# Kernel optimization log

Hardware: AMD Instinct MI355X
Metric: run time of the kernel (lower is better)

## Reference

```python
import jax, jax.numpy as jnp
import numpy as np

N, E, F_IN, F_OUT = 8192, 1024, 256, 256


def setup_inputs() -> dict:
    key = jax.random.key(0)
    k1, k2, k3, k4 = jax.random.split(key, 4)
    X = jax.random.normal(k1, (N, F_IN), dtype=jnp.float32)
    # binary incidence matrix: node i belongs to hyperedge j with p=0.05
    H = (jax.random.uniform(k2, (N, E)) < 0.05).astype(jnp.float32)
    W = jax.random.normal(k3, (F_OUT, F_IN), dtype=jnp.float32) * (1.0 / np.sqrt(F_IN))
    b = jax.random.normal(k4, (F_OUT,), dtype=jnp.float32) * 0.01
    return {"X": X, "H": H, "W": W, "b": b}


def reference(X, H, W, b):
    # Dv = diag(row sums of H), De = diag(col sums of H)
    dv = jnp.sum(H, axis=1)                      # [N] node degrees
    de = jnp.sum(H, axis=0)                      # [E] edge degrees
    dv_inv_sqrt = 1.0 / jnp.sqrt(dv)             # inv of sqrt(Dv) (diagonal)
    de_inv = 1.0 / de                            # inv of De (diagonal)
    # diagonal matrices realized as broadcast scalings (same math, no N x N).
    Xs = X * dv_inv_sqrt[:, None]
    M = H.T @ Xs                                 # H^T (...)          [E, F]
    M = M * de_inv[:, None]                      # De^-1 (...)        [E, F]
    X_new = (H @ M) * dv_inv_sqrt[:, None]       # Dv^-1/2 H (...)    [N, F]
    return X_new @ W.T + b                       # nn.Linear
```

## Files before the change

### kernel.cpp

```cpp
#include <hip/hip_runtime.h>
#include <hip/hip_bf16.h>
#include <stdint.h>

typedef __attribute__((ext_vector_type(8))) short bf16x8;
typedef __attribute__((ext_vector_type(4))) float f32x4;
typedef __attribute__((ext_vector_type(4))) unsigned int u32x4;
typedef __attribute__((ext_vector_type(2))) unsigned int u32x2;
typedef unsigned short u16;
typedef unsigned int u32;
typedef unsigned char u8;
typedef unsigned long long u64;

#define N_NODES 8192
#define N_EDGES 1024
#define F_DIM   256
#define NMAX 128

__device__ __forceinline__ u16 f2bf(float f) {
    union { float f; u32 u; } v; v.f = f;
    u32 u = v.u;
    u = (u + 0x7FFFu + ((u >> 16) & 1u)) >> 16;
    return (u16)u;
}
__device__ __forceinline__ float bflo(u32 p) {
    union { u32 u; float f; } v; v.u = p << 16; return v.f;
}
__device__ __forceinline__ float bfhi(u32 p) {
    union { u32 u; float f; } v; v.u = p & 0xffff0000u; return v.f;
}

__device__ __forceinline__ void async16(const u16* g, u16* l) {
    __builtin_amdgcn_global_load_lds(
        (const __attribute__((address_space(1))) u32*)(const void*)g,
        (__attribute__((address_space(3))) u32*)(void*)l, 16, 0, 0);
}

__device__ __forceinline__ bf16x8 expand8(u32 byte) {
    union { u32 u[4]; bf16x8 v; } r;
#pragma unroll
    for (int i = 0; i < 4; ++i)
        r.u[i] = (((byte >> (2 * i)) & 1u) ? 0x3F80u : 0u)
               | (((byte >> (2 * i + 1)) & 1u) ? 0x3F800000u : 0u);
    return r.v;
}

__global__ __launch_bounds__(512) void prep(
    const float* __restrict__ H, const float* __restrict__ X,
    const float* __restrict__ W,
    float* __restrict__ dv, u16* __restrict__ nlist,
    u16* __restrict__ Xst, u32* __restrict__ HbTs, u16* __restrict__ Wb) {
    __shared__ u16 hmask[32][64];
    __shared__ u16 tT[256][34];
    const int tid = threadIdx.x;
    const int wv = tid >> 6;
    const int lane = tid & 63;
    const int blk = blockIdx.x;
    const int n0 = blk * 32 + wv * 4;

    f32x4 hv[4][4], xv[4];
#pragma unroll
    for (int r = 0; r < 4; ++r) {
        const int n = n0 + r;
#pragma unroll
        for (int q = 0; q < 4; ++q)
            hv[r][q] = *(const f32x4*)(&H[(size_t)n * N_EDGES + q * 256 + lane * 4]);
        xv[r] = *(const f32x4*)(&X[(size_t)n * F_DIM + lane * 4]);
    }

    if (wv == 7) {
        const f32x4 w = *(const f32x4*)(&W[(size_t)blk * F_DIM + lane * 4]);
        u32x2 pk;
        pk[0] = (u32)f2bf(w[0]) | ((u32)f2bf(w[1]) << 16);
        pk[1] = (u32)f2bf(w[2]) | ((u32)f2bf(w[3]) << 16);
        *(u32x2*)(&Wb[(size_t)blk * F_DIM + lane * 4]) = pk;
    }

#pragma unroll
    for (int r = 0; r < 4; ++r) {
        const int n = n0 + r;
        u32 m16 = 0u;
#pragma unroll
        for (int q = 0; q < 4; ++q)
#pragma unroll
            for (int j = 0; j < 4; ++j)
                m16 |= ((hv[r][q][j] != 0.f) ? 1u : 0u) << (q * 4 + j);
        hmask[wv * 4 + r][lane] = (u16)m16;
        const u32 cl = (u32)__popc(m16);
        u32 x = cl;
#pragma unroll
        for (int d = 1; d < 64; d <<= 1) {
            const u32 t = __shfl_up(x, d, 64);
            if (lane >= d) x += t;
        }
        const u32 total = __shfl(x, 63, 64);
        u32 pos = x - cl;
        u16* nrow = &nlist[(size_t)n * NMAX];
        u32 m = m16;
        while (m) {
            const int bidx = __builtin_ctz(m);
            m &= m - 1;
            const int col = ((bidx >> 2) << 8) + lane * 4 + (bidx & 3);
            if (pos < NMAX) nrow[pos] = (u16)col;
            ++pos;
        }
        if (lane == 0) dv[n] = (float)total;
        const float s = rsqrtf((float)total);
#pragma unroll
        for (int j = 0; j < 4; ++j)
            tT[lane * 4 + j][wv * 4 + r] = f2bf(xv[r][j] * s);
    }
    __syncthreads();
    {
        u32x2 st;
#pragma unroll
        for (int eo = 0; eo < 2; ++eo) {
            const int e = tid * 2 + eo;
            const int widx = (e & 255) >> 2;
            const int bit = ((e >> 8) << 2) + (e & 3);
            u32 w = 0u;
#pragma unroll
            for (int r = 0; r < 32; ++r)
                w |= (u32)((hmask[r][widx] >> bit) & 1u) << r;
            st[eo] = w;
        }
        *(u32x2*)(&HbTs[(size_t)blk * N_EDGES + tid * 2]) = st;
    }
    {
        const int f = tid & 255, half = tid >> 8;
        const u32* src = (const u32*)(&tT[f][half * 16]);
        u32x4 a, b2;
#pragma unroll
        for (int i = 0; i < 4; ++i) { a[i] = src[i]; b2[i] = src[i + 4]; }
        u16* dst = &Xst[(size_t)f * N_NODES + blk * 32 + half * 16];
        *(u32x4*)dst = a;
        *(u32x4*)(dst + 8) = b2;
    }
}

__global__ __launch_bounds__(512) void gemm1(
    const u16* __restrict__ Xst, const u32* __restrict__ HbTs,
    u16* __restrict__ Mb) {
    __shared__ __align__(16) u8 smem[65536];
    __shared__ float cnts[8][2][16];
    const int tid = threadIdx.x;
    const int wv = tid >> 6, lane = tid & 63;
    const int f0 = ((int)blockIdx.x & 7) * 32;
    const int e0 = ((int)blockIdx.x >> 3) * 32;
    const int row16 = lane & 15, quad = lane >> 4;
    const int srow = lane & 15, schunk = lane >> 4;
    u16* myBs = (u16*)(smem + wv * 8192);
    const int kbase = wv * 1024;

    f32x4 acc[2][2] = {};
    u32 cnt0 = 0, cnt1 = 0;
    u32 wA[2][2], wB[2][2];

    auto STAGE = [&](int it, int buf) {
        __builtin_amdgcn_sched_barrier(0);
        const int k0 = kbase + it * 64;
#pragma unroll
        for (int tn = 0; tn < 2; ++tn)
#pragma unroll
            for (int ks = 0; ks < 2; ++ks)
                async16(Xst + (size_t)(f0 + tn * 16 + srow) * N_NODES + k0 + ks * 32 + schunk * 8,
                        myBs + buf * 2048 + (tn * 2 + ks) * 512);
    };
    auto LOADW = [&](int it, u32 (&w)[2][2]) {
        const int k0 = kbase + it * 64;
#pragma unroll
        for (int tm = 0; tm < 2; ++tm)
#pragma unroll
            for (int ks = 0; ks < 2; ++ks)
                w[tm][ks] = HbTs[(size_t)((k0 >> 5) + ks) * N_EDGES + e0 + tm * 16 + row16];
    };
    auto COMPUTE = [&](int buf, u32 (&w)[2][2]) {
        asm volatile("s_waitcnt vmcnt(4)" ::: "memory");
        __builtin_amdgcn_sched_barrier(0);
#pragma unroll
        for (int ks = 0; ks < 2; ++ks) {
            bf16x8 bfr[2];
#pragma unroll
            for (int tn = 0; tn < 2; ++tn)
                bfr[tn] = *(const bf16x8*)(myBs + buf * 2048 + (tn * 2 + ks) * 512 + lane * 8);
#pragma unroll
            for (int tm = 0; tm < 2; ++tm) {
                const u32 byte = (w[tm][ks] >> (quad * 8)) & 0xFFu;
                if (tm == 0) cnt0 += (u32)__popc(byte); else cnt1 += (u32)__popc(byte);
                const bf16x8 af = expand8(byte);
#pragma unroll
                for (int tn = 0; tn < 2; ++tn)
                    acc[tm][tn] = __builtin_amdgcn_mfma_f32_16x16x32_bf16(
                        af, bfr[tn], acc[tm][tn], 0, 0, 0);
            }
        }
    };

    STAGE(0, 0);
    LOADW(0, wA);
    for (int i = 0; i < 8; ++i) {
        STAGE(2 * i + 1, 1);
        LOADW(2 * i + 1, wB);
        COMPUTE(0, wA);
        const int nxt = (2 * i + 2 < 16) ? (2 * i + 2) : 15;
        STAGE(nxt, 0);
        LOADW(nxt, wA);
        COMPUTE(1, wB);
    }

    cnt0 += __shfl_down(cnt0, 32, 64); cnt0 += __shfl_down(cnt0, 16, 64);
    cnt1 += __shfl_down(cnt1, 32, 64); cnt1 += __shfl_down(cnt1, 16, 64);
    if (lane < 16) {
        cnts[wv][0][lane] = (float)cnt0;
        cnts[wv][1][lane] = (float)cnt1;
    }
    __syncthreads();
    {
        float* redf = (float*)smem;
        float* my = &redf[(size_t)(wv * 64 + lane) * 17];
#pragma unroll
        for (int tm = 0; tm < 2; ++tm)
#pragma unroll
            for (int tn = 0; tn < 2; ++tn)
#pragma unroll
                for (int r = 0; r < 4; ++r)
                    my[tm * 8 + tn * 4 + r] = acc[tm][tn][r];
    }
    __syncthreads();
    {
        const float* redf = (const float*)smem;
#pragma unroll
        for (int h = 0; h < 2; ++h) {
            const int idx = tid + h * 512;
            const int el = idx >> 5, fl = idx & 31;
            const int tm = el >> 4, q = (el >> 2) & 3, r = el & 3;
            const int tn = fl >> 4, r16 = fl & 15;
            const int srcl = q * 16 + r16;
            const int j = tm * 8 + tn * 4 + r;
            float s = 0.f, de = 0.f;
#pragma unroll
            for (int w = 0; w < 8; ++w) {
                s += redf[(size_t)(w * 64 + srcl) * 17 + j];
                de += cnts[w][tm][el & 15];
            }
            Mb[(size_t)(e0 + el) * F_DIM + f0 + fl] = f2bf(s / de);
        }
    }
}

__global__ __launch_bounds__(512) void spmm2w(
    const u16* __restrict__ Mb, const float* __restrict__ dv,
    const u16* __restrict__ nlist, const u16* __restrict__ Wb,
    const float* __restrict__ bias, float* __restrict__ out) {
    __shared__ u16 nl[8 * NMAX];
    __shared__ u16 Yb[8][264];
    const int tid = threadIdx.x;
    const int wv = tid >> 6;
    const int lane = tid & 63;
    const int n0 = blockIdx.x * 8;
    ((u32*)nl)[tid] = ((const u32*)&nlist[(size_t)n0 * NMAX])[tid];
    __syncthreads();
    const int half = lane >> 5, l32 = lane & 31;
    const int n = n0 + wv;
    const float dvn = dv[n];
    const int cnt = min((int)dvn, NMAX);
    const u16* lt = &nl[wv * NMAX];
    float a[8] = {};
    const int npairs = (cnt + 1) >> 1;
#pragma unroll 8
    for (int p = 0; p < npairs; ++p) {
        const int idx0 = 2 * p + half;
        const int idx = min(idx0, cnt - 1);
        const float msk = (idx0 < cnt) ? 1.f : 0.f;
        const int e = lt[idx];
        const u32x4 pk = *(const u32x4*)(&Mb[(size_t)e * F_DIM + l32 * 8]);
        a[0] = fmaf(bflo(pk[0]), msk, a[0]); a[1] = fmaf(bfhi(pk[0]), msk, a[1]);
        a[2] = fmaf(bflo(pk[1]), msk, a[2]); a[3] = fmaf(bfhi(pk[1]), msk, a[3]);
        a[4] = fmaf(bflo(pk[2]), msk, a[4]); a[5] = fmaf(bfhi(pk[2]), msk, a[5]);
        a[6] = fmaf(bflo(pk[3]), msk, a[6]); a[7] = fmaf(bfhi(pk[3]), msk, a[7]);
    }
#pragma unroll
    for (int k = 0; k < 8; ++k) a[k] += __shfl_xor(a[k], 32, 64);
    const float s = rsqrtf(dvn);
    if (half == 0) {
        u32x4 pk;
        pk[0] = (u32)f2bf(a[0] * s) | ((u32)f2bf(a[1] * s) << 16);
        pk[1] = (u32)f2bf(a[2] * s) | ((u32)f2bf(a[3] * s) << 16);
        pk[2] = (u32)f2bf(a[4] * s) | ((u32)f2bf(a[5] * s) << 16);
        pk[3] = (u32)f2bf(a[6] * s) | ((u32)f2bf(a[7] * s) << 16);
        *(u32x4*)(&Yb[wv][l32 * 8]) = pk;
    }
    __syncthreads();
    const int row16 = lane & 15, quad = lane >> 4;
    f32x4 acc[2] = {};
    for (int ko = 0; ko < 256; ko += 32) {
        bf16x8 af = {};
        if (row16 < 8)
            af = *(const bf16x8*)(&Yb[row16][ko + quad * 8]);
#pragma unroll
        for (int tn = 0; tn < 2; ++tn) {
            const int j = wv * 32 + tn * 16 + row16;
            const bf16x8 bf = *(const bf16x8*)(&Wb[(size_t)j * F_DIM + ko + quad * 8]);
            acc[tn] = __builtin_amdgcn_mfma_f32_16x16x32_bf16(af, bf, acc[tn], 0, 0, 0);
        }
    }
#pragma unroll
    for (int tn = 0; tn < 2; ++tn) {
        const int col = wv * 32 + tn * 16 + row16;
        const float bc = bias[col];
#pragma unroll
        for (int r2 = 0; r2 < 4; ++r2) {
            const int row = quad * 4 + r2;
            if (row < 8)
                out[(size_t)(n0 + row) * F_DIM + col] = acc[tn][r2] + bc;
        }
    }
}

extern "C" void kernel_launch(void* const* d_in, const int* in_sizes, int n_in,
                              void* d_out, int out_size, void* d_ws, size_t ws_size,
                              hipStream_t stream) {
    (void)in_sizes; (void)n_in; (void)out_size; (void)ws_size;
    const float* X = (const float*)d_in[0];
    const float* H = (const float*)d_in[1];
    const float* W = (const float*)d_in[2];
    const float* b = (const float*)d_in[3];
    float* out = (float*)d_out;

    char* ws = (char*)d_ws;
    float* dv    = (float*)(ws);
    u32*   HbTs  = (u32*)(ws + 0x10000);
    u16*   nlist = (u16*)(ws + 0x110000);
    u16*   Xst   = (u16*)(ws + 0x310000);
    u16*   Mb    = (u16*)(ws + 0x710000);
    u16*   Wb    = (u16*)(ws + 0x790000);

    prep<<<256, 512, 0, stream>>>(H, X, W, dv, nlist, Xst, HbTs, Wb);
    gemm1<<<256, 512, 0, stream>>>(Xst, HbTs, Mb);
    spmm2w<<<N_NODES / 8, 512, 0, stream>>>(Mb, dv, nlist, Wb, b, out);
}
```

Measured before the change: 138.4 us.

## Reassociate linear layer before hypergraph propagation and replace gather SpMM with bitmask MFMA GEMM

The Linear weight is applied first (Z = W·Xs), so the two incidence products run on already-projected features. The final propagation becomes a dense MFMA GEMM over a node-major bit-packed incidence matrix instead of a per-node neighbor-list gather, and the neighbor-list construction in prep is removed. This adds a fourth kernel and an extra 8192x256 bf16 intermediate in exchange for regular, coalesced MFMA work and no degree cap in the second product.

```diff
diff --git a/kernel.cpp b/kernel.cpp
--- a/kernel.cpp
+++ b/kernel.cpp
@@ -14,7 +14,6 @@
 #define N_NODES 8192
 #define N_EDGES 1024
 #define F_DIM   256
-#define NMAX 128
 
 __device__ __forceinline__ u16 f2bf(float f) {
     union { float f; u32 u; } v; v.f = f;
@@ -22,12 +21,6 @@
     u = (u + 0x7FFFu + ((u >> 16) & 1u)) >> 16;
     return (u16)u;
 }
-__device__ __forceinline__ float bflo(u32 p) {
-    union { u32 u; float f; } v; v.u = p << 16; return v.f;
-}
-__device__ __forceinline__ float bfhi(u32 p) {
-    union { u32 u; float f; } v; v.u = p & 0xffff0000u; return v.f;
-}
 
 __device__ __forceinline__ void async16(const u16* g, u16* l) {
     __builtin_amdgcn_global_load_lds(
@@ -47,10 +40,9 @@
 __global__ __launch_bounds__(512) void prep(
     const float* __restrict__ H, const float* __restrict__ X,
     const float* __restrict__ W,
-    float* __restrict__ dv, u16* __restrict__ nlist,
-    u16* __restrict__ Xst, u32* __restrict__ HbTs, u16* __restrict__ Wb) {
-    __shared__ u16 hmask[32][64];
-    __shared__ u16 tT[256][34];
+    float* __restrict__ dv, u16* __restrict__ Xsb,
+    u32* __restrict__ HbTs, u32* __restrict__ HbN, u16* __restrict__ Wb) {
+    __shared__ u16 hmask[32][68];
     const int tid = threadIdx.x;
     const int wv = tid >> 6;
     const int lane = tid & 63;
@@ -85,29 +77,15 @@
             for (int j = 0; j < 4; ++j)
                 m16 |= ((hv[r][q][j] != 0.f) ? 1u : 0u) << (q * 4 + j);
         hmask[wv * 4 + r][lane] = (u16)m16;
-        const u32 cl = (u32)__popc(m16);
-        u32 x = cl;
-#pragma unroll
-        for (int d = 1; d < 64; d <<= 1) {
-            const u32 t = __shfl_up(x, d, 64);
-            if (lane >= d) x += t;
-        }
-        const u32 total = __shfl(x, 63, 64);
-        u32 pos = x - cl;
-        u16* nrow = &nlist[(size_t)n * NMAX];
-        u32 m = m16;
-        while (m) {
-            const int bidx = __builtin_ctz(m);
-            m &= m - 1;
-            const int col = ((bidx >> 2) << 8) + lane * 4 + (bidx & 3);
-            if (pos < NMAX) nrow[pos] = (u16)col;
-            ++pos;
-        }
-        if (lane == 0) dv[n] = (float)total;
-        const float s = rsqrtf((float)total);
-#pragma unroll
-        for (int j = 0; j < 4; ++j)
-            tT[lane * 4 + j][wv * 4 + r] = f2bf(xv[r][j] * s);
+        u32 s = (u32)__popc(m16);
+#pragma unroll
+        for (int d = 1; d < 64; d <<= 1) s += __shfl_xor(s, d, 64);
+        if (lane == 0) dv[n] = (float)s;
+        const float sc = rsqrtf((float)s);
+        u32x2 pk;
+        pk[0] = (u32)f2bf(xv[r][0] * sc) | ((u32)f2bf(xv[r][1] * sc) << 16);
+        pk[1] = (u32)f2bf(xv[r][2] * sc) | ((u32)f2bf(xv[r][3] * sc) << 16);
+        *(u32x2*)(&Xsb[(size_t)n * F_DIM + lane * 4]) = pk;
     }
     __syncthreads();
     {
@@ -126,20 +104,89 @@
         *(u32x2*)(&HbTs[(size_t)blk * N_EDGES + tid * 2]) = st;
     }
     {
-        const int f = tid & 255, half = tid >> 8;
-        const u32* src = (const u32*)(&tT[f][half * 16]);
-        u32x4 a, b2;
-#pragma unroll
-        for (int i = 0; i < 4; ++i) { a[i] = src[i]; b2[i] = src[i + 4]; }
-        u16* dst = &Xst[(size_t)f * N_NODES + blk * 32 + half * 16];
-        *(u32x4*)dst = a;
-        *(u32x4*)(dst + 8) = b2;
-    }
-}
-
-__global__ __launch_bounds__(512) void gemm1(
-    const u16* __restrict__ Xst, const u32* __restrict__ HbTs,
-    u16* __restrict__ Mb) {
+        const int r = tid & 31;
+        const int wec = tid >> 5;
+#pragma unroll
+        for (int wo = 0; wo < 2; ++wo) {
+            const int we = wec + wo * 16;
+            const int q = we >> 3, l0 = (we & 7) * 8;
+            const u32x2 a = *(const u32x2*)(&hmask[r][l0]);
+            const u32x2 b2 = *(const u32x2*)(&hmask[r][l0 + 4]);
+            const u32 sh = q * 4;
+            u32 w = ((a[0] >> sh) & 0xFu)
+                  | (((a[0] >> (16 + sh)) & 0xFu) << 4)
+                  | (((a[1] >> sh) & 0xFu) << 8)
+                  | (((a[1] >> (16 + sh)) & 0xFu) << 12)
+                  | (((b2[0] >> sh) & 0xFu) << 16)
+                  | (((b2[0] >> (16 + sh)) & 0xFu) << 20)
+                  | (((b2[1] >> sh) & 0xFu) << 24)
+                  | (((b2[1] >> (16 + sh)) & 0xFu) << 28);
+            HbN[(size_t)we * N_NODES + blk * 32 + r] = w;
+        }
+    }
+}
+
+__global__ __launch_bounds__(256) void gemmZ(
+    const u16* __restrict__ Wb, const u16* __restrict__ Xsb,
+    u16* __restrict__ Zt) {
+    __shared__ __align__(16) u16 As[64 * 64];
+    __shared__ __align__(16) u16 Bs[64 * 64];
+    const int tid = threadIdx.x;
+    const int lane = tid & 63;
+    const int wave = tid >> 6;
+    const int wm = wave >> 1, wn = wave & 1;
+    const int row16 = lane & 15;
+    const int quad = lane >> 4;
+    const int row0 = blockIdx.y * 64;
+    const int col0 = blockIdx.x * 64;
+    const int srow = lane >> 3;
+    const int scol = (lane & 7) * 8;
+    const u16* gA0 = Wb + (size_t)(row0 + wave * 16 + srow) * F_DIM + scol;
+    const u16* gB0 = Xsb + (size_t)(col0 + wave * 16 + srow) * F_DIM + scol;
+    const size_t rstep8 = (size_t)8 * F_DIM;
+    u16* lA0 = &As[(wave * 16) * 64];
+    u16* lB0 = &Bs[(wave * 16) * 64];
+
+    f32x4 acc[2][2] = {};
+    for (int k = 0; k < 256; k += 64) {
+        async16(gA0 + k, lA0);
+        async16(gA0 + k + rstep8, lA0 + 8 * 64);
+        async16(gB0 + k, lB0);
+        async16(gB0 + k + rstep8, lB0 + 8 * 64);
+        __syncthreads();
+#pragma unroll
+        for (int ks = 0; ks < 2; ++ks) {
+            bf16x8 af[2], bfr[2];
+#pragma unroll
+            for (int t = 0; t < 2; ++t) {
+                af[t]  = *(const bf16x8*)(&As[(wm * 32 + t * 16 + row16) * 64 + ks * 32 + quad * 8]);
+                bfr[t] = *(const bf16x8*)(&Bs[(wn * 32 + t * 16 + row16) * 64 + ks * 32 + quad * 8]);
+            }
+#pragma unroll
+            for (int tm = 0; tm < 2; tm++)
+#pragma unroll
+                for (int tn = 0; tn < 2; tn++)
+                    acc[tm][tn] = __builtin_amdgcn_mfma_f32_16x16x32_bf16(
+                        af[tm], bfr[tn], acc[tm][tn], 0, 0, 0);
+        }
+        __syncthreads();
+    }
+#pragma unroll
+    for (int tm = 0; tm < 2; tm++)
+#pragma unroll
+        for (int tn = 0; tn < 2; tn++) {
+            const int col = col0 + wn * 32 + tn * 16 + row16;
+#pragma unroll
+            for (int r = 0; r < 4; r++) {
+                const int row = row0 + wm * 32 + tm * 16 + quad * 4 + r;
+                Zt[(size_t)row * N_NODES + col] = f2bf(acc[tm][tn][r]);
+            }
+        }
+}
+
+__global__ __launch_bounds__(512) void gemmM2(
+    const u16* __restrict__ Zt, const u32* __restrict__ HbTs,
+    u16* __restrict__ M2t) {
     __shared__ __align__(16) u8 smem[65536];
     __shared__ float cnts[8][2][16];
     const int tid = threadIdx.x;
@@ -162,7 +209,7 @@
         for (int tn = 0; tn < 2; ++tn)
 #pragma unroll
             for (int ks = 0; ks < 2; ++ks)
-                async16(Xst + (size_t)(f0 + tn * 16 + srow) * N_NODES + k0 + ks * 32 + schunk * 8,
+                async16(Zt + (size_t)(f0 + tn * 16 + srow) * N_NODES + k0 + ks * 32 + schunk * 8,
                         myBs + buf * 2048 + (tn * 2 + ks) * 512);
     };
     auto LOADW = [&](int it, u32 (&w)[2][2]) {
@@ -231,7 +278,7 @@
 #pragma unroll
         for (int h = 0; h < 2; ++h) {
             const int idx = tid + h * 512;
-            const int el = idx >> 5, fl = idx & 31;
+            const int fl = idx >> 5, el = idx & 31;
             const int tm = el >> 4, q = (el >> 2) & 3, r = el & 3;
             const int tn = fl >> 4, r16 = fl & 15;
             const int srcl = q * 16 + r16;
@@ -242,78 +289,86 @@
                 s += redf[(size_t)(w * 64 + srcl) * 17 + j];
                 de += cnts[w][tm][el & 15];
             }
-            Mb[(size_t)(e0 + el) * F_DIM + f0 + fl] = f2bf(s / de);
-        }
-    }
-}
-
-__global__ __launch_bounds__(512) void spmm2w(
-    const u16* __restrict__ Mb, const float* __restrict__ dv,
-    const u16* __restrict__ nlist, const u16* __restrict__ Wb,
-    const float* __restrict__ bias, float* __restrict__ out) {
-    __shared__ u16 nl[8 * NMAX];
-    __shared__ u16 Yb[8][264];
+            M2t[(size_t)(f0 + fl) * N_EDGES + e0 + el] = f2bf(s / de);
+        }
+    }
+}
+
+__global__ __launch_bounds__(512) void gemmOUT(
+    const u16* __restrict__ M2t, const u32* __restrict__ HbN,
+    const float* __restrict__ dv, const float* __restrict__ bias,
+    float* __restrict__ out) {
+    __shared__ __align__(16) u16 Bs[32 * 1028];
     const int tid = threadIdx.x;
-    const int wv = tid >> 6;
-    const int lane = tid & 63;
-    const int n0 = blockIdx.x * 8;
-    ((u32*)nl)[tid] = ((const u32*)&nlist[(size_t)n0 * NMAX])[tid];
+    const int wv = tid >> 6, lane = tid & 63;
+    const int row16 = lane & 15, quad = lane >> 4;
+    const int j0 = ((int)blockIdx.x & 7) * 32;
+    const int ng = ((int)blockIdx.x >> 3) * 256 + wv * 32;
+
+#pragma unroll
+    for (int rr = 0; rr < 4; ++rr) {
+        const int jr = wv * 4 + rr;
+#pragma unroll
+        for (int c = 0; c < 2; ++c)
+            async16(M2t + (size_t)(j0 + jr) * N_EDGES + c * 512 + lane * 8,
+                    &Bs[jr * 1028 + c * 512]);
+    }
     __syncthreads();
-    const int half = lane >> 5, l32 = lane & 31;
-    const int n = n0 + wv;
-    const float dvn = dv[n];
-    const int cnt = min((int)dvn, NMAX);
-    const u16* lt = &nl[wv * NMAX];
-    float a[8] = {};
-    const int npairs = (cnt + 1) >> 1;
-#pragma unroll 8
-    for (int p = 0; p < npairs; ++p) {
-        const int idx0 = 2 * p + half;
-        const int idx = min(idx0, cnt - 1);
-        const float msk = (idx0 < cnt) ? 1.f : 0.f;
-        const int e = lt[idx];
-        const u32x4 pk = *(const u32x4*)(&Mb[(size_t)e * F_DIM + l32 * 8]);
-        a[0] = fmaf(bflo(pk[0]), msk, a[0]); a[1] = fmaf(bfhi(pk[0]), msk, a[1]);
-        a[2] = fmaf(bflo(pk[1]), msk, a[2]); a[3] = fmaf(bfhi(pk[1]), msk, a[3]);
-        a[4] = fmaf(bflo(pk[2]), msk, a[4]); a[5] = fmaf(bfhi(pk[2]), msk, a[5]);
-        a[6] = fmaf(bflo(pk[3]), msk, a[6]); a[7] = fmaf(bfhi(pk[3]), msk, a[7]);
-    }
-#pragma unroll
-    for (int k = 0; k < 8; ++k) a[k] += __shfl_xor(a[k], 32, 64);
-    const float s = rsqrtf(dvn);
-    if (half == 0) {
-        u32x4 pk;
-        pk[0] = (u32)f2bf(a[0] * s) | ((u32)f2bf(a[1] * s) << 16);
-        pk[1] = (u32)f2bf(a[2] * s) | ((u32)f2bf(a[3] * s) << 16);
-        pk[2] = (u32)f2bf(a[4] * s) | ((u32)f2bf(a[5] * s) << 16);
-        pk[3] = (u32)f2bf(a[6] * s) | ((u32)f2bf(a[7] * s) << 16);
-        *(u32x4*)(&Yb[wv][l32 * 8]) = pk;
-    }
-    __syncthreads();
-    const int row16 = lane & 15, quad = lane >> 4;
-    f32x4 acc[2] = {};
-    for (int ko = 0; ko < 256; ko += 32) {
-        bf16x8 af = {};
-        if (row16 < 8)
-            af = *(const bf16x8*)(&Yb[row16][ko + quad * 8]);
+
+    f32x4 acc[2][2] = {};
+    u32 wA[2][2], wB[2][2];
+    auto LOADW = [&](int it, u32 (&w)[2][2]) {
+#pragma unroll
+        for (int tm = 0; tm < 2; ++tm)
+#pragma unroll
+            for (int ks = 0; ks < 2; ++ks)
+                w[tm][ks] = HbN[(size_t)(it * 2 + ks) * N_NODES + ng + tm * 16 + row16];
+    };
+    auto COMPUTE = [&](int it, u32 (&w)[2][2]) {
+#pragma unroll
+        for (int ks = 0; ks < 2; ++ks) {
+            bf16x8 bfr[2];
+#pragma unroll
+            for (int tn = 0; tn < 2; ++tn) {
+                const int base = (tn * 16 + row16) * 1028 + it * 64 + ks * 32 + quad * 8;
+                union { u32x2 lo_hi[2]; bf16x8 v; } u;
+                u.lo_hi[0] = *(const u32x2*)(&Bs[base]);
+                u.lo_hi[1] = *(const u32x2*)(&Bs[base + 4]);
+                bfr[tn] = u.v;
+            }
+#pragma unroll
+            for (int tm = 0; tm < 2; ++tm) {
+                const u32 byte = (w[tm][ks] >> (quad * 8)) & 0xFFu;
+                const bf16x8 af = expand8(byte);
+#pragma unroll
+                for (int tn = 0; tn < 2; ++tn)
+                    acc[tm][tn] = __builtin_amdgcn_mfma_f32_16x16x32_bf16(
+                        af, bfr[tn], acc[tm][tn], 0, 0, 0);
+            }
+        }
+    };
+
+    LOADW(0, wA);
+    for (int i = 0; i < 8; ++i) {
+        LOADW(2 * i + 1, wB);
+        COMPUTE(2 * i, wA);
+        const int nxt = (2 * i + 2 < 16) ? (2 * i + 2) : 15;
+        LOADW(nxt, wA);
+        COMPUTE(2 * i + 1, wB);
+    }
+
+#pragma unroll
+    for (int tm = 0; tm < 2; ++tm)
 #pragma unroll
         for (int tn = 0; tn < 2; ++tn) {
-            const int j = wv * 32 + tn * 16 + row16;
-            const bf16x8 bf = *(const bf16x8*)(&Wb[(size_t)j * F_DIM + ko + quad * 8]);
-            acc[tn] = __builtin_amdgcn_mfma_f32_16x16x32_bf16(af, bf, acc[tn], 0, 0, 0);
-        }
-    }
-#pragma unroll
-    for (int tn = 0; tn < 2; ++tn) {
-        const int col = wv * 32 + tn * 16 + row16;
-        const float bc = bias[col];
-#pragma unroll
-        for (int r2 = 0; r2 < 4; ++r2) {
-            const int row = quad * 4 + r2;
-            if (row < 8)
-                out[(size_t)(n0 + row) * F_DIM + col] = acc[tn][r2] + bc;
-        }
-    }
+            const int col = j0 + tn * 16 + row16;
+            const float bc = bias[col];
+#pragma unroll
+            for (int r = 0; r < 4; ++r) {
+                const int n = ng + tm * 16 + quad * 4 + r;
+                out[(size_t)n * F_DIM + col] = acc[tm][tn][r] * rsqrtf(dv[n]) + bc;
+            }
+        }
 }
 
 extern "C" void kernel_launch(void* const* d_in, const int* in_sizes, int n_in,
@@ -327,14 +382,16 @@
     float* out = (float*)d_out;
 
     char* ws = (char*)d_ws;
-    float* dv    = (float*)(ws);
-    u32*   HbTs  = (u32*)(ws + 0x10000);
-    u16*   nlist = (u16*)(ws + 0x110000);
-    u16*   Xst   = (u16*)(ws + 0x310000);
-    u16*   Mb    = (u16*)(ws + 0x710000);
-    u16*   Wb    = (u16*)(ws + 0x790000);
-
-    prep<<<256, 512, 0, stream>>>(H, X, W, dv, nlist, Xst, HbTs, Wb);
-    gemm1<<<256, 512, 0, stream>>>(Xst, HbTs, Mb);
-    spmm2w<<<N_NODES / 8, 512, 0, stream>>>(Mb, dv, nlist, Wb, b, out);
-}
+    float* dv   = (float*)(ws);
+    u32*   HbTs = (u32*)(ws + 0x10000);
+    u32*   HbN  = (u32*)(ws + 0x110000);
+    u16*   Wb   = (u16*)(ws + 0x210000);
+    u16*   Xsb  = (u16*)(ws + 0x230000);
+    u16*   Zt   = (u16*)(ws + 0x630000);
+    u16*   M2t  = (u16*)(ws + 0xA30000);
+
+    prep<<<256, 512, 0, stream>>>(H, X, W, dv, Xsb, HbTs, HbN, Wb);
+    gemmZ<<<dim3(128, 4), 256, 0, stream>>>(Wb, Xsb, Zt);
+    gemmM2<<<256, 512, 0, stream>>>(Zt, HbTs, M2t);
+    gemmOUT<<<256, 512, 0, stream>>>(M2t, HbN, dv, b, out);
+}
```

New measurement: 121.8 us. -12.0%, faster.
